# Performance work log

Hardware: AMD Instinct MI355X
Metric: run time of the kernel (lower is better)

Reference implementation:

```python
import jax, jax.numpy as jnp
import numpy as np
import math

N = 65536
IN_FEATURES = 64
OUT_FEATURES = 64
N_MODES = 32
N_BASIS = 1 + 2 * N_MODES


def setup_inputs() -> dict:
    key = jax.random.key(0)
    k1, k2 = jax.random.split(key)
    x = jax.random.normal(k1, (N, IN_FEATURES), dtype=jnp.float32)
    coeffs = jax.random.normal(k2, (OUT_FEATURES, IN_FEATURES, N_BASIS), dtype=jnp.float32) * 0.1
    bias = jnp.zeros((OUT_FEATURES,), dtype=jnp.float32)
    return {"x": x, "coeffs": coeffs, "bias": bias}


def reference(x, coeffs, bias):
    # freqs: [modes] = (1..modes) * pi
    freqs = jnp.arange(1, N_MODES + 1, dtype=x.dtype) * jnp.asarray(math.pi, dtype=x.dtype)
    x_flat = x.reshape(-1, IN_FEATURES)                      # [n, i]
    angles = x_flat[..., None] * freqs                       # [n, i, m]
    ones = jnp.ones(x_flat.shape + (1,), dtype=x.dtype)      # [n, i, 1]
    basis = jnp.concatenate([ones, jnp.sin(angles), jnp.cos(angles)], axis=-1)  # [n, i, b]
    out = jnp.einsum('oib,nib->no', coeffs, basis) + bias    # [n, o]
    return out.reshape(*x.shape[:-1], OUT_FEATURES)
```

## Files before the change

kernel.cpp:

```cpp
#include <hip/hip_runtime.h>
#include <hip/hip_bf16.h>


typedef __bf16 bf16x8 __attribute__((ext_vector_type(8)));
typedef float  f32x4  __attribute__((ext_vector_type(4)));
typedef float  f32x16 __attribute__((ext_vector_type(16)));

#define PI_F 3.14159265358979323846f

__global__ __launch_bounds__(256) void fkan_repack(
    const float* __restrict__ coeffs, const float* __restrict__ bias,
    __bf16* __restrict__ Bp, float* __restrict__ bias2) {
  int gid  = blockIdx.x * 256 + threadIdx.x;
  int lane = gid & 63;
  int frag = gid >> 6;
  int m  = frag >> 4;
  int kc = (frag >> 1) & 7;
  int cc = frag & 1;
  int o  = cc * 32 + (lane & 31);
  int kq = lane >> 5;

  bf16x8 v;
  #pragma unroll
  for (int t = 0; t < 8; ++t) {
    int i = kc * 8 + kq * 4 + (t >> 1);
    int b = (t & 1) ? (33 + m) : (1 + m);
    v[t] = (__bf16)coeffs[(o * 64 + i) * 65 + b];
  }
  *(bf16x8*)(Bp + (size_t)frag * 512 + lane * 8) = v;

  if (blockIdx.x == 0 && threadIdx.x < 64) {
    int oo = threadIdx.x;
    float s = bias[oo];
    #pragma unroll 4
    for (int ii = 0; ii < 64; ++ii) s += coeffs[(oo * 64 + ii) * 65 + 0];
    bias2[oo] = s;
  }
}

__device__ __forceinline__ void stage_slice(const __bf16* __restrict__ Bp,
                                            __bf16* dst, int m, int wave,
                                            int lane) {
  const char* g = (const char*)Bp + (size_t)m * 16384 + wave * 4096 + lane * 16;
  char* l = (char*)dst + wave * 4096;
  #pragma unroll
  for (int r = 0; r < 4; ++r) {
    __builtin_amdgcn_global_load_lds(
        (const __attribute__((address_space(1))) void*)(g + r * 1024),
        (__attribute__((address_space(3))) void*)(l + r * 1024), 16, 0, 0);
  }
}

__global__ __launch_bounds__(256, 2) void fkan_main(
    const float* __restrict__ x, const __bf16* __restrict__ Bp,
    const float* __restrict__ bias2, float* __restrict__ out) {
  __shared__ __bf16 Bs[2][8192];

  int tid  = threadIdx.x;
  int wave = tid >> 6;
  int lane = tid & 63;
  int kq   = lane >> 5;
  int cl   = lane & 31;
  int row  = blockIdx.x * 128 + wave * 32 + cl;

  float T[32], sp[32], cp[32], sc[32], cc_[32];
  const float* xrow = x + (size_t)row * 64 + kq * 4;
  #pragma unroll
  for (int kc = 0; kc < 8; ++kc) {
    f32x4 v = *(const f32x4*)(xrow + kc * 8);
    #pragma unroll
    for (int e = 0; e < 4; ++e) {
      int p = kc * 4 + e;
      float ss, cs;
      __sincosf(PI_F * v[e], &ss, &cs);
      T[p] = 2.0f * cs;
      sc[p] = ss;  cc_[p] = cs;
      sp[p] = 0.f; cp[p] = 1.f;
    }
  }

  f32x16 acc[2];
  #pragma unroll
  for (int c2 = 0; c2 < 2; ++c2)
    #pragma unroll
    for (int r = 0; r < 16; ++r) acc[c2][r] = 0.f;

  stage_slice(Bp, &Bs[0][0], 0, wave, lane);
  __syncthreads();

  for (int m = 0; m < 32; m += 2) {
    if (m + 1 < 32) stage_slice(Bp, &Bs[1][0], m + 1, wave, lane);
    #pragma unroll
    for (int kc = 0; kc < 8; ++kc) {
      bf16x8 af;
      #pragma unroll
      for (int e = 0; e < 4; ++e) {
        af[2 * e]     = (__bf16)sc[kc * 4 + e];
        af[2 * e + 1] = (__bf16)cc_[kc * 4 + e];
      }
      #pragma unroll
      for (int c2 = 0; c2 < 2; ++c2) {
        bf16x8 bf = *(const bf16x8*)(&Bs[0][(kc * 2 + c2) * 512 + lane * 8]);
        acc[c2] = __builtin_amdgcn_mfma_f32_32x32x16_bf16(af, bf, acc[c2],
                                                          0, 0, 0);
      }
    }
    #pragma unroll
    for (int p = 0; p < 32; ++p) {
      sp[p] = fmaf(T[p], sc[p], -sp[p]);
      cp[p] = fmaf(T[p], cc_[p], -cp[p]);
    }
    __syncthreads();

    if (m + 2 < 32) stage_slice(Bp, &Bs[0][0], m + 2, wave, lane);
    #pragma unroll
    for (int kc = 0; kc < 8; ++kc) {
      bf16x8 af;
      #pragma unroll
      for (int e = 0; e < 4; ++e) {
        af[2 * e]     = (__bf16)sp[kc * 4 + e];
        af[2 * e + 1] = (__bf16)cp[kc * 4 + e];
      }
      #pragma unroll
      for (int c2 = 0; c2 < 2; ++c2) {
        bf16x8 bf = *(const bf16x8*)(&Bs[1][(kc * 2 + c2) * 512 + lane * 8]);
        acc[c2] = __builtin_amdgcn_mfma_f32_32x32x16_bf16(af, bf, acc[c2],
                                                          0, 0, 0);
      }
    }
    #pragma unroll
    for (int p = 0; p < 32; ++p) {
      sc[p]  = fmaf(T[p], sp[p], -sc[p]);
      cc_[p] = fmaf(T[p], cp[p], -cc_[p]);
    }
    __syncthreads();
  }

  float* orow = out + (size_t)(blockIdx.x * 128 + wave * 32) * 64;
  #pragma unroll
  for (int c2 = 0; c2 < 2; ++c2) {
    float b2 = bias2[c2 * 32 + cl];
    #pragma unroll
    for (int r = 0; r < 16; ++r) {
      int ro = (r & 3) + 8 * (r >> 2) + 4 * kq;
      orow[(size_t)ro * 64 + c2 * 32 + cl] = acc[c2][r] + b2;
    }
  }
}

extern "C" void kernel_launch(void* const* d_in, const int* in_sizes, int n_in,
                              void* d_out, int out_size, void* d_ws, size_t ws_size,
                              hipStream_t stream) {
  const float* x      = (const float*)d_in[0];
  const float* coeffs = (const float*)d_in[1];
  const float* bias   = (const float*)d_in[2];
  float* out = (float*)d_out;

  __bf16* Bp   = (__bf16*)d_ws;
  float* bias2 = (float*)((char*)d_ws + 512 * 1024);

  int n_rows = in_sizes[0] / 64;

  fkan_repack<<<128, 256, 0, stream>>>(coeffs, bias, Bp, bias2);
  fkan_main<<<n_rows / 128, 256, 0, stream>>>(x, Bp, bias2, out);
}
```

Baseline: 112.1 us.

## Deepen LDS staging to four buffers with vmcnt waits and single barrier

Switches the coefficient staging from a double buffer to a four-slot ring, keeping two mode slices in flight. Each step uses an explicit vmcnt wait plus one raw s_barrier in place of two __syncthreads per iteration. The sin/cos recurrence state is packed into paired vectors and the unrolled loop is bounded with unroll 1. This doubles LDS use to 64KB per block, which may limit occupancy, and relies on the compiler not reordering memory ops around the hand-written waits.

```diff
diff --git a/kernel.cpp b/kernel.cpp
--- a/kernel.cpp
+++ b/kernel.cpp
@@ -3,6 +3,7 @@
 
 
 typedef __bf16 bf16x8 __attribute__((ext_vector_type(8)));
+typedef float  f32x2  __attribute__((ext_vector_type(2)));
 typedef float  f32x4  __attribute__((ext_vector_type(4)));
 typedef float  f32x16 __attribute__((ext_vector_type(16)));
 
@@ -51,10 +52,45 @@
   }
 }
 
+#define ASM_VMCNT(N) asm volatile("s_waitcnt vmcnt(" #N ")" ::: "memory")
+
+__device__ __forceinline__ void block_barrier() {
+  asm volatile("" ::: "memory");
+  __builtin_amdgcn_s_barrier();
+  asm volatile("" ::: "memory");
+}
+
+__device__ __forceinline__ void compute_mode(const __bf16* bsrc, int lane,
+                                             const f32x2* cur, f32x2* nxt,
+                                             const float* T, f32x16* acc) {
+  #pragma unroll
+  for (int kc = 0; kc < 8; ++kc) {
+    bf16x8 af;
+    #pragma unroll
+    for (int e = 0; e < 4; ++e) {
+      af[2 * e]     = (__bf16)cur[kc * 4 + e][0];
+      af[2 * e + 1] = (__bf16)cur[kc * 4 + e][1];
+    }
+    #pragma unroll
+    for (int c2 = 0; c2 < 2; ++c2) {
+      bf16x8 bf = *(const bf16x8*)(bsrc + (kc * 2 + c2) * 512 + lane * 8);
+      acc[c2] = __builtin_amdgcn_mfma_f32_32x32x16_bf16(af, bf, acc[c2],
+                                                        0, 0, 0);
+    }
+  }
+  #pragma unroll
+  for (int p = 0; p < 32; ++p) {
+    f32x2 n;
+    n[0] = fmaf(T[p], cur[p][0], -nxt[p][0]);
+    n[1] = fmaf(T[p], cur[p][1], -nxt[p][1]);
+    nxt[p] = n;
+  }
+}
+
 __global__ __launch_bounds__(256, 2) void fkan_main(
     const float* __restrict__ x, const __bf16* __restrict__ Bp,
     const float* __restrict__ bias2, float* __restrict__ out) {
-  __shared__ __bf16 Bs[2][8192];
+  __shared__ __bf16 Bs[4][8192];
 
   int tid  = threadIdx.x;
   int wave = tid >> 6;
@@ -63,7 +99,8 @@
   int cl   = lane & 31;
   int row  = blockIdx.x * 128 + wave * 32 + cl;
 
-  float T[32], sp[32], cp[32], sc[32], cc_[32];
+  float T[32];
+  f32x2 cur[32], prv[32];
   const float* xrow = x + (size_t)row * 64 + kq * 4;
   #pragma unroll
   for (int kc = 0; kc < 8; ++kc) {
@@ -74,8 +111,8 @@
       float ss, cs;
       __sincosf(PI_F * v[e], &ss, &cs);
       T[p] = 2.0f * cs;
-      sc[p] = ss;  cc_[p] = cs;
-      sp[p] = 0.f; cp[p] = 1.f;
+      cur[p][0] = ss;  cur[p][1] = cs;
+      prv[p][0] = 0.f; prv[p][1] = 1.f;
     }
   }
 
@@ -86,55 +123,34 @@
     for (int r = 0; r < 16; ++r) acc[c2][r] = 0.f;
 
   stage_slice(Bp, &Bs[0][0], 0, wave, lane);
-  __syncthreads();
+  stage_slice(Bp, &Bs[1][0], 1, wave, lane);
 
-  for (int m = 0; m < 32; m += 2) {
-    if (m + 1 < 32) stage_slice(Bp, &Bs[1][0], m + 1, wave, lane);
-    #pragma unroll
-    for (int kc = 0; kc < 8; ++kc) {
-      bf16x8 af;
-      #pragma unroll
-      for (int e = 0; e < 4; ++e) {
-        af[2 * e]     = (__bf16)sc[kc * 4 + e];
-        af[2 * e + 1] = (__bf16)cc_[kc * 4 + e];
-      }
-      #pragma unroll
-      for (int c2 = 0; c2 < 2; ++c2) {
-        bf16x8 bf = *(const bf16x8*)(&Bs[0][(kc * 2 + c2) * 512 + lane * 8]);
-        acc[c2] = __builtin_amdgcn_mfma_f32_32x32x16_bf16(af, bf, acc[c2],
-                                                          0, 0, 0);
-      }
-    }
-    #pragma unroll
-    for (int p = 0; p < 32; ++p) {
-      sp[p] = fmaf(T[p], sc[p], -sp[p]);
-      cp[p] = fmaf(T[p], cc_[p], -cp[p]);
-    }
-    __syncthreads();
+  #pragma unroll 1
+  for (int mm = 0; mm < 28; mm += 2) {
+    stage_slice(Bp, &Bs[(mm + 2) & 3][0], mm + 2, wave, lane);
+    ASM_VMCNT(8);
+    block_barrier();
+    compute_mode(&Bs[mm & 3][0], lane, cur, prv, T, acc);
 
-    if (m + 2 < 32) stage_slice(Bp, &Bs[0][0], m + 2, wave, lane);
-    #pragma unroll
-    for (int kc = 0; kc < 8; ++kc) {
-      bf16x8 af;
-      #pragma unroll
-      for (int e = 0; e < 4; ++e) {
-        af[2 * e]     = (__bf16)sp[kc * 4 + e];
-        af[2 * e + 1] = (__bf16)cp[kc * 4 + e];
-      }
-      #pragma unroll
-      for (int c2 = 0; c2 < 2; ++c2) {
-        bf16x8 bf = *(const bf16x8*)(&Bs[1][(kc * 2 + c2) * 512 + lane * 8]);
-        acc[c2] = __builtin_amdgcn_mfma_f32_32x32x16_bf16(af, bf, acc[c2],
-                                                          0, 0, 0);
-      }
-    }
-    #pragma unroll
-    for (int p = 0; p < 32; ++p) {
-      sc[p]  = fmaf(T[p], sp[p], -sc[p]);
-      cc_[p] = fmaf(T[p], cp[p], -cc_[p]);
-    }
-    __syncthreads();
+    stage_slice(Bp, &Bs[(mm + 3) & 3][0], mm + 3, wave, lane);
+    ASM_VMCNT(8);
+    block_barrier();
+    compute_mode(&Bs[(mm + 1) & 3][0], lane, prv, cur, T, acc);
   }
+
+  stage_slice(Bp, &Bs[2][0], 30, wave, lane);
+  ASM_VMCNT(8);  block_barrier();
+  compute_mode(&Bs[0][0], lane, cur, prv, T, acc);
+
+  stage_slice(Bp, &Bs[3][0], 31, wave, lane);
+  ASM_VMCNT(8);  block_barrier();
+  compute_mode(&Bs[1][0], lane, prv, cur, T, acc);
+
+  ASM_VMCNT(4);  block_barrier();
+  compute_mode(&Bs[2][0], lane, cur, prv, T, acc);
+
+  ASM_VMCNT(0);  block_barrier();
+  compute_mode(&Bs[3][0], lane, prv, cur, T, acc);
 
   float* orow = out + (size_t)(blockIdx.x * 128 + wave * 32) * 64;
   #pragma unroll
```

Measured after the change: 118.0 us. 1.05x slower.

## Stage two harmonic slices per barrier and hoist Chebyshev recurrence before MFMAs

Applied to the files above, without the earlier changes.

Each pipeline phase now loads two frequency slices into a larger double-buffered LDS tile, which halves the number of block-wide barriers. Inside a phase, the recurrence for the next harmonic is computed before the MFMAs that use the current one, so the VALU work can overlap with matrix instructions. The loop is kept rolled (unroll 1), with the last phases peeled. LDS use doubles to 64 KB per block, which may limit occupancy under the two-blocks-per-CU launch bound.

```diff
diff --git a/kernel.cpp b/kernel.cpp
--- a/kernel.cpp
+++ b/kernel.cpp
@@ -38,23 +38,72 @@
   }
 }
 
-__device__ __forceinline__ void stage_slice(const __bf16* __restrict__ Bp,
-                                            __bf16* dst, int m, int wave,
-                                            int lane) {
-  const char* g = (const char*)Bp + (size_t)m * 16384 + wave * 4096 + lane * 16;
+__device__ __forceinline__ void stage_pair(const __bf16* __restrict__ Bp,
+                                           __bf16* dst, int ph, int wave,
+                                           int lane) {
+  const char* g = (const char*)Bp + (size_t)ph * 32768 + wave * 4096 + lane * 16;
   char* l = (char*)dst + wave * 4096;
   #pragma unroll
   for (int r = 0; r < 4; ++r) {
     __builtin_amdgcn_global_load_lds(
         (const __attribute__((address_space(1))) void*)(g + r * 1024),
         (__attribute__((address_space(3))) void*)(l + r * 1024), 16, 0, 0);
+    __builtin_amdgcn_global_load_lds(
+        (const __attribute__((address_space(1))) void*)(g + 16384 + r * 1024),
+        (__attribute__((address_space(3))) void*)(l + 16384 + r * 1024),
+        16, 0, 0);
+  }
+}
+
+__device__ __forceinline__ void phase_compute(const __bf16* buf, int lane,
+    const float* T, float* sA, float* cA, float* sB, float* cB,
+    f32x16* acc) {
+  #pragma unroll
+  for (int p = 0; p < 32; ++p) {
+    sB[p] = fmaf(T[p], sA[p], -sB[p]);
+    cB[p] = fmaf(T[p], cA[p], -cB[p]);
+  }
+  #pragma unroll
+  for (int kc = 0; kc < 8; ++kc) {
+    bf16x8 af;
+    #pragma unroll
+    for (int e = 0; e < 4; ++e) {
+      af[2 * e]     = (__bf16)sA[kc * 4 + e];
+      af[2 * e + 1] = (__bf16)cA[kc * 4 + e];
+    }
+    #pragma unroll
+    for (int c2 = 0; c2 < 2; ++c2) {
+      bf16x8 bfv = *(const bf16x8*)(buf + (kc * 2 + c2) * 512 + lane * 8);
+      acc[c2] = __builtin_amdgcn_mfma_f32_32x32x16_bf16(af, bfv, acc[c2],
+                                                        0, 0, 0);
+    }
+  }
+  #pragma unroll
+  for (int kc = 0; kc < 8; ++kc) {
+    bf16x8 af;
+    #pragma unroll
+    for (int e = 0; e < 4; ++e) {
+      af[2 * e]     = (__bf16)sB[kc * 4 + e];
+      af[2 * e + 1] = (__bf16)cB[kc * 4 + e];
+    }
+    #pragma unroll
+    for (int c2 = 0; c2 < 2; ++c2) {
+      bf16x8 bfv = *(const bf16x8*)(buf + 8192 + (kc * 2 + c2) * 512 + lane * 8);
+      acc[c2] = __builtin_amdgcn_mfma_f32_32x32x16_bf16(af, bfv, acc[c2],
+                                                        0, 0, 0);
+    }
+  }
+  #pragma unroll
+  for (int p = 0; p < 32; ++p) {
+    sA[p] = fmaf(T[p], sB[p], -sA[p]);
+    cA[p] = fmaf(T[p], cB[p], -cA[p]);
   }
 }
 
 __global__ __launch_bounds__(256, 2) void fkan_main(
     const float* __restrict__ x, const __bf16* __restrict__ Bp,
     const float* __restrict__ bias2, float* __restrict__ out) {
-  __shared__ __bf16 Bs[2][8192];
+  __shared__ __bf16 Bs[2][16384];
 
   int tid  = threadIdx.x;
   int wave = tid >> 6;
@@ -85,56 +134,24 @@
     #pragma unroll
     for (int r = 0; r < 16; ++r) acc[c2][r] = 0.f;
 
-  stage_slice(Bp, &Bs[0][0], 0, wave, lane);
+  stage_pair(Bp, &Bs[0][0], 0, wave, lane);
   __syncthreads();
 
-  for (int m = 0; m < 32; m += 2) {
-    if (m + 1 < 32) stage_slice(Bp, &Bs[1][0], m + 1, wave, lane);
-    #pragma unroll
-    for (int kc = 0; kc < 8; ++kc) {
-      bf16x8 af;
-      #pragma unroll
-      for (int e = 0; e < 4; ++e) {
-        af[2 * e]     = (__bf16)sc[kc * 4 + e];
-        af[2 * e + 1] = (__bf16)cc_[kc * 4 + e];
-      }
-      #pragma unroll
-      for (int c2 = 0; c2 < 2; ++c2) {
-        bf16x8 bf = *(const bf16x8*)(&Bs[0][(kc * 2 + c2) * 512 + lane * 8]);
-        acc[c2] = __builtin_amdgcn_mfma_f32_32x32x16_bf16(af, bf, acc[c2],
-                                                          0, 0, 0);
-      }
-    }
-    #pragma unroll
-    for (int p = 0; p < 32; ++p) {
-      sp[p] = fmaf(T[p], sc[p], -sp[p]);
-      cp[p] = fmaf(T[p], cc_[p], -cp[p]);
-    }
+  #pragma unroll 1
+  for (int ph = 0; ph < 14; ph += 2) {
+    stage_pair(Bp, &Bs[1][0], ph + 1, wave, lane);
+    phase_compute(&Bs[0][0], lane, T, sc, cc_, sp, cp, acc);
     __syncthreads();
 
-    if (m + 2 < 32) stage_slice(Bp, &Bs[0][0], m + 2, wave, lane);
-    #pragma unroll
-    for (int kc = 0; kc < 8; ++kc) {
-      bf16x8 af;
-      #pragma unroll
-      for (int e = 0; e < 4; ++e) {
-        af[2 * e]     = (__bf16)sp[kc * 4 + e];
-        af[2 * e + 1] = (__bf16)cp[kc * 4 + e];
-      }
-      #pragma unroll
-      for (int c2 = 0; c2 < 2; ++c2) {
-        bf16x8 bf = *(const bf16x8*)(&Bs[1][(kc * 2 + c2) * 512 + lane * 8]);
-        acc[c2] = __builtin_amdgcn_mfma_f32_32x32x16_bf16(af, bf, acc[c2],
-                                                          0, 0, 0);
-      }
-    }
-    #pragma unroll
-    for (int p = 0; p < 32; ++p) {
-      sc[p]  = fmaf(T[p], sp[p], -sc[p]);
-      cc_[p] = fmaf(T[p], cp[p], -cc_[p]);
-    }
+    stage_pair(Bp, &Bs[0][0], ph + 2, wave, lane);
+    phase_compute(&Bs[1][0], lane, T, sc, cc_, sp, cp, acc);
     __syncthreads();
   }
+
+  stage_pair(Bp, &Bs[1][0], 15, wave, lane);
+  phase_compute(&Bs[0][0], lane, T, sc, cc_, sp, cp, acc);
+  __syncthreads();
+  phase_compute(&Bs[1][0], lane, T, sc, cc_, sp, cp, acc);
 
   float* orow = out + (size_t)(blockIdx.x * 128 + wave * 32) * 64;
   #pragma unroll
```

After: 114.4 us. +2.1%, slower.

## Split K across wave pairs to halve registers and double occupancy

Applied to the files above, without the earlier changes.

Each 32-row tile is now handled by two waves, each covering half of the input features (32 of 64). This halves the per-thread Chebyshev recurrence state and lets blocks grow to 512 threads with launch bounds targeting 4 blocks per CU. The partial accumulators are summed through LDS at the end. The main loop is also left un-unrolled and the tail peeled. The cost is an extra LDS reduction, an extra barrier, and duplicated recurrence bookkeeping per wave pair.

```diff
diff --git a/kernel.cpp b/kernel.cpp
--- a/kernel.cpp
+++ b/kernel.cpp
@@ -38,39 +38,66 @@
   }
 }
 
-__device__ __forceinline__ void stage_slice(const __bf16* __restrict__ Bp,
-                                            __bf16* dst, int m, int wave,
-                                            int lane) {
-  const char* g = (const char*)Bp + (size_t)m * 16384 + wave * 4096 + lane * 16;
-  char* l = (char*)dst + wave * 4096;
+__device__ __forceinline__ void stage_mode(const __bf16* __restrict__ Bp,
+                                           __bf16* dst, int m, int tid) {
+  const char* g = (const char*)Bp + (size_t)m * 16384 + tid * 16;
+  char* l = (char*)dst + tid * 16;
+  __builtin_amdgcn_global_load_lds(
+      (const __attribute__((address_space(1))) void*)g,
+      (__attribute__((address_space(3))) void*)l, 16, 0, 0);
+  __builtin_amdgcn_global_load_lds(
+      (const __attribute__((address_space(1))) void*)(g + 8192),
+      (__attribute__((address_space(3))) void*)(l + 8192), 16, 0, 0);
+}
+
+__device__ __forceinline__ void mode_compute(const __bf16* buf, int lane,
+    int h, const float* T, const float* sA, const float* cA,
+    float* sN, float* cN, f32x16* acc) {
   #pragma unroll
-  for (int r = 0; r < 4; ++r) {
-    __builtin_amdgcn_global_load_lds(
-        (const __attribute__((address_space(1))) void*)(g + r * 1024),
-        (__attribute__((address_space(3))) void*)(l + r * 1024), 16, 0, 0);
+  for (int kcr = 0; kcr < 4; ++kcr) {
+    bf16x8 af;
+    #pragma unroll
+    for (int e = 0; e < 4; ++e) {
+      af[2 * e]     = (__bf16)sA[kcr * 4 + e];
+      af[2 * e + 1] = (__bf16)cA[kcr * 4 + e];
+    }
+    int kc = 4 * h + kcr;
+    #pragma unroll
+    for (int c2 = 0; c2 < 2; ++c2) {
+      bf16x8 bfv = *(const bf16x8*)(buf + (kc * 2 + c2) * 512 + lane * 8);
+      acc[c2] = __builtin_amdgcn_mfma_f32_32x32x16_bf16(af, bfv, acc[c2],
+                                                        0, 0, 0);
+    }
+  }
+  #pragma unroll
+  for (int p = 0; p < 16; ++p) {
+    sN[p] = fmaf(T[p], sA[p], -sN[p]);
+    cN[p] = fmaf(T[p], cA[p], -cN[p]);
   }
 }
 
-__global__ __launch_bounds__(256, 2) void fkan_main(
+__global__ __launch_bounds__(512, 4) void fkan_main(
     const float* __restrict__ x, const __bf16* __restrict__ Bp,
     const float* __restrict__ bias2, float* __restrict__ out) {
   __shared__ __bf16 Bs[2][8192];
 
   int tid  = threadIdx.x;
   int wave = tid >> 6;
+  int rt   = wave >> 1;
+  int h    = wave & 1;
   int lane = tid & 63;
   int kq   = lane >> 5;
   int cl   = lane & 31;
-  int row  = blockIdx.x * 128 + wave * 32 + cl;
+  int row  = blockIdx.x * 128 + rt * 32 + cl;
 
-  float T[32], sp[32], cp[32], sc[32], cc_[32];
-  const float* xrow = x + (size_t)row * 64 + kq * 4;
+  float T[16], sp[16], cp[16], sc[16], cc_[16];
+  const float* xrow = x + (size_t)row * 64 + h * 32 + kq * 4;
   #pragma unroll
-  for (int kc = 0; kc < 8; ++kc) {
-    f32x4 v = *(const f32x4*)(xrow + kc * 8);
+  for (int kcr = 0; kcr < 4; ++kcr) {
+    f32x4 v = *(const f32x4*)(xrow + kcr * 8);
     #pragma unroll
     for (int e = 0; e < 4; ++e) {
-      int p = kc * 4 + e;
+      int p = kcr * 4 + e;
       float ss, cs;
       __sincosf(PI_F * v[e], &ss, &cs);
       T[p] = 2.0f * cs;
@@ -85,65 +112,48 @@
     #pragma unroll
     for (int r = 0; r < 16; ++r) acc[c2][r] = 0.f;
 
-  stage_slice(Bp, &Bs[0][0], 0, wave, lane);
+  stage_mode(Bp, &Bs[0][0], 0, tid);
   __syncthreads();
 
-  for (int m = 0; m < 32; m += 2) {
-    if (m + 1 < 32) stage_slice(Bp, &Bs[1][0], m + 1, wave, lane);
-    #pragma unroll
-    for (int kc = 0; kc < 8; ++kc) {
-      bf16x8 af;
-      #pragma unroll
-      for (int e = 0; e < 4; ++e) {
-        af[2 * e]     = (__bf16)sc[kc * 4 + e];
-        af[2 * e + 1] = (__bf16)cc_[kc * 4 + e];
-      }
-      #pragma unroll
-      for (int c2 = 0; c2 < 2; ++c2) {
-        bf16x8 bf = *(const bf16x8*)(&Bs[0][(kc * 2 + c2) * 512 + lane * 8]);
-        acc[c2] = __builtin_amdgcn_mfma_f32_32x32x16_bf16(af, bf, acc[c2],
-                                                          0, 0, 0);
-      }
-    }
-    #pragma unroll
-    for (int p = 0; p < 32; ++p) {
-      sp[p] = fmaf(T[p], sc[p], -sp[p]);
-      cp[p] = fmaf(T[p], cc_[p], -cp[p]);
-    }
+  #pragma unroll 1
+  for (int m = 0; m < 30; m += 2) {
+    stage_mode(Bp, &Bs[1][0], m + 1, tid);
+    mode_compute(&Bs[0][0], lane, h, T, sc, cc_, sp, cp, acc);
     __syncthreads();
 
-    if (m + 2 < 32) stage_slice(Bp, &Bs[0][0], m + 2, wave, lane);
-    #pragma unroll
-    for (int kc = 0; kc < 8; ++kc) {
-      bf16x8 af;
-      #pragma unroll
-      for (int e = 0; e < 4; ++e) {
-        af[2 * e]     = (__bf16)sp[kc * 4 + e];
-        af[2 * e + 1] = (__bf16)cp[kc * 4 + e];
-      }
-      #pragma unroll
-      for (int c2 = 0; c2 < 2; ++c2) {
-        bf16x8 bf = *(const bf16x8*)(&Bs[1][(kc * 2 + c2) * 512 + lane * 8]);
-        acc[c2] = __builtin_amdgcn_mfma_f32_32x32x16_bf16(af, bf, acc[c2],
-                                                          0, 0, 0);
-      }
-    }
-    #pragma unroll
-    for (int p = 0; p < 32; ++p) {
-      sc[p]  = fmaf(T[p], sp[p], -sc[p]);
-      cc_[p] = fmaf(T[p], cp[p], -cc_[p]);
-    }
+    stage_mode(Bp, &Bs[0][0], m + 2, tid);
+    mode_compute(&Bs[1][0], lane, h, T, sp, cp, sc, cc_, acc);
     __syncthreads();
   }
 
-  float* orow = out + (size_t)(blockIdx.x * 128 + wave * 32) * 64;
-  #pragma unroll
-  for (int c2 = 0; c2 < 2; ++c2) {
-    float b2 = bias2[c2 * 32 + cl];
+  stage_mode(Bp, &Bs[1][0], 31, tid);
+  mode_compute(&Bs[0][0], lane, h, T, sc, cc_, sp, cp, acc);
+  __syncthreads();
+  mode_compute(&Bs[1][0], lane, h, T, sp, cp, sc, cc_, acc);
+  __syncthreads();
+
+  float* red = (float*)&Bs[0][0];
+  if (h == 1) {
     #pragma unroll
-    for (int r = 0; r < 16; ++r) {
-      int ro = (r & 3) + 8 * (r >> 2) + 4 * kq;
-      orow[(size_t)ro * 64 + c2 * 32 + cl] = acc[c2][r] + b2;
+    for (int r = 0; r < 32; ++r)
+      red[rt * 2048 + r * 64 + lane] = acc[r >> 4][r & 15];
+  }
+  __syncthreads();
+
+  if (h == 0) {
+    #pragma unroll
+    for (int r = 0; r < 32; ++r)
+      acc[r >> 4][r & 15] += red[rt * 2048 + r * 64 + lane];
+
+    float* orow = out + (size_t)(blockIdx.x * 128 + rt * 32) * 64;
+    #pragma unroll
+    for (int c2 = 0; c2 < 2; ++c2) {
+      float b2 = bias2[c2 * 32 + cl];
+      #pragma unroll
+      for (int r = 0; r < 16; ++r) {
+        int ro = (r & 3) + 8 * (r >> 2) + 4 * kq;
+        orow[(size_t)ro * 64 + c2 * 32 + cl] = acc[c2][r] + b2;
+      }
     }
   }
 }
@@ -162,5 +172,5 @@
   int n_rows = in_sizes[0] / 64;
 
   fkan_repack<<<128, 256, 0, stream>>>(coeffs, bias, Bp, bias2);
-  fkan_main<<<n_rows / 128, 256, 0, stream>>>(x, Bp, bias2, out);
+  fkan_main<<<n_rows / 128, 512, 0, stream>>>(x, Bp, bias2, out);
 }
```

New measurement: 353.8 us. +215.6%, slower.
